# Performance work log

Hardware: AMD Instinct MI355X
Metric: run time of the kernel (lower is better)

## Reference

```python
import jax, jax.numpy as jnp
import numpy as np

NHEADS = 8
LN_EPS = 1e-5

def _layer_norm(x, g, b):
    mu = jnp.mean(x, axis=-1, keepdims=True)
    var = jnp.mean((x - mu) ** 2, axis=-1, keepdims=True)
    return (x - mu) * jax.lax.rsqrt(var + LN_EPS) * g + b

def setup_inputs() -> dict:
    key = jax.random.key(0)
    ks = jax.random.split(key, 12)
    B, L, D = 8, 1024, 512
    F = 2 * D  # ffn_dim = 2*dim
    std = 0.01  # init_weights: Linear weights ~ N(0, 0.01), biases zero
    inp = {
        'query': jax.random.normal(ks[0], (B, L, D), dtype=jnp.float32),
        'q_mask': jnp.ones((B, L), dtype=jnp.int32),
        'wq': jax.random.normal(ks[1], (D, D), dtype=jnp.float32) * std,
        'bq': jnp.zeros((D,), dtype=jnp.float32),
        'wk': jax.random.normal(ks[2], (D, D), dtype=jnp.float32) * std,
        'bk': jnp.zeros((D,), dtype=jnp.float32),
        'wv': jax.random.normal(ks[3], (D, D), dtype=jnp.float32) * std,
        'bv': jnp.zeros((D,), dtype=jnp.float32),
        'wo': jax.random.normal(ks[4], (D, D), dtype=jnp.float32) * std,
        'bo': jnp.zeros((D,), dtype=jnp.float32),
        'ln1_g': jnp.ones((D,), dtype=jnp.float32),
        'ln1_b': jnp.zeros((D,), dtype=jnp.float32),
        'w1': jax.random.normal(ks[5], (D, F), dtype=jnp.float32) * std,
        'b1': jnp.zeros((F,), dtype=jnp.float32),
        'w2': jax.random.normal(ks[6], (F, D), dtype=jnp.float32) * std,
        'b2': jnp.zeros((D,), dtype=jnp.float32),
        'ln2_g': jnp.ones((D,), dtype=jnp.float32),
        'ln2_b': jnp.zeros((D,), dtype=jnp.float32),
    }
    return inp

def reference(query, q_mask, wq, bq, wk, bk, wv, bv, wo, bo, ln1_g, ln1_b, w1, b1, w2, b2, ln2_g, ln2_b):
    B, L, D = query.shape
    H = NHEADS
    dh = D // H
    residual = query
    # projections (dropout in eval mode -> identity)
    q = query @ wq + bq
    k = query @ wk + bk
    v = query @ wv + bv
    # faithful to torch .view(batch*nheads, -1, dim_head) (no head transpose)
    q = q.reshape(B * H, L, dh)
    k = k.reshape(B * H, L, dh)
    v = v.reshape(B * H, L, dh)
    # faithful to torch mask.repeat(nheads, 1) -> tile along batch dim
    mf = q_mask.astype(jnp.float32)
    qm = jnp.tile(mf, (H, 1))  # [B*H, L]
    km = qm
    mask = qm[:, :, None] * km[:, None, :]  # [B*H, L, L] outer product
    scores = jnp.einsum('bqd,bkd->bqk', q, k) / np.sqrt(dh).astype(np.float32)
    A = jnp.where(mask == 0, 0.0, jnp.exp(scores))  # masked_fill(-inf).exp()
    A_sum = jnp.maximum(jnp.sum(A, axis=-1, keepdims=True), 1.0)
    attn = A / A_sum
    context = jnp.einsum('bqk,bkd->bqd', attn, v).reshape(B, L, H * dh)
    out = context @ wo + bo
    out = _layer_norm(residual + out, ln1_g, ln1_b)
    # positional-wise FFN: Linear -> ReLU -> Linear, residual + LayerNorm
    ffn = jax.nn.relu(out @ w1 + b1) @ w2 + b2
    out2 = _layer_norm(out + ffn, ln2_g, ln2_b)
    return (out2, q_mask, query, query, q_mask)
```

## Files before the change

### kernel.cpp

```cpp
#include <hip/hip_runtime.h>
#include <hip/hip_bf16.h>

typedef __hip_bfloat16 bf16;
typedef __attribute__((ext_vector_type(4))) float f32x4;
typedef __attribute__((ext_vector_type(8))) short s16x8;
typedef __attribute__((ext_vector_type(4))) short s16x4;

#define MFMA(a, b, c) __builtin_amdgcn_mfma_f32_16x16x32_bf16((a), (b), (c), 0, 0, 0)

__device__ __forceinline__ void g2l16(const bf16* g, bf16* l) {
  __builtin_amdgcn_global_load_lds((const __attribute__((address_space(1))) void*)g,
                                   (__attribute__((address_space(3))) void*)l,
                                   16, 0, 0);
}
__device__ __forceinline__ bf16 cvt_bf(float f) { return __float2bfloat16(f); }
__device__ __forceinline__ float bf2f(bf16 h) { return __bfloat162float(h); }

__global__ __launch_bounds__(256)
void prep2_k(const float* __restrict__ query, const int* __restrict__ qmask,
             const float* __restrict__ wq, const float* __restrict__ wk,
             const float* __restrict__ wv, const float* __restrict__ wo,
             const float* __restrict__ w1, const float* __restrict__ w2,
             bf16* __restrict__ wqkvT, bf16* __restrict__ woT,
             bf16* __restrict__ w1T, bf16* __restrict__ w2T,
             bf16* __restrict__ qb, float* __restrict__ out)
{
  __shared__ float tl[32][33];
  const int bid = blockIdx.x;
  if (bid < 2048) {
    const float* W; bf16* Wt; int K, N, tile;
    if (bid < 768)        { int s = bid >> 8; W = s==0?wq:(s==1?wk:wv);
                            Wt = wqkvT + s*262144; K = 512; N = 512; tile = bid & 255; }
    else if (bid < 1024)  { W = wo; Wt = woT; K = 512;  N = 512;  tile = bid - 768; }
    else if (bid < 1536)  { W = w1; Wt = w1T; K = 512;  N = 1024; tile = bid - 1024; }
    else                  { W = w2; Wt = w2T; K = 1024; N = 512;  tile = bid - 1536; }
    const int nx = N >> 5;
    const int n0 = (tile % nx) * 32, k0 = (tile / nx) * 32;
    const int tx = threadIdx.x & 31, ty = threadIdx.x >> 5;
#pragma unroll
    for (int i = 0; i < 32; i += 8)
      tl[ty + i][tx] = W[(size_t)(k0 + ty + i) * N + n0 + tx];
    __syncthreads();
#pragma unroll
    for (int i = 0; i < 32; i += 8)
      Wt[(size_t)(n0 + ty + i) * K + k0 + tx] = cvt_bf(tl[tx][ty + i]);
  } else if (bid < 4096) {
    const int i = (bid - 2048) * 2048 + threadIdx.x * 8;
    float4 a = *(const float4*)(query + i);
    float4 b = *(const float4*)(query + i + 4);
    union { bf16 h[8]; s16x8 v; } u;
    u.h[0] = cvt_bf(a.x); u.h[1] = cvt_bf(a.y); u.h[2] = cvt_bf(a.z); u.h[3] = cvt_bf(a.w);
    u.h[4] = cvt_bf(b.x); u.h[5] = cvt_bf(b.y); u.h[6] = cvt_bf(b.z); u.h[7] = cvt_bf(b.w);
    *(s16x8*)(qb + i) = u.v;
    float* o1 = out + 4202496 + i;
    float* o2 = out + 8396800 + i;
    *(float4*)o1 = a; *(float4*)(o1 + 4) = b;
    *(float4*)o2 = a; *(float4*)(o2 + 4) = b;
  } else {
    const int j = (bid - 4096) * 256 + threadIdx.x;
    const float v = (float)qmask[j];
    out[4194304 + j] = v;
    out[12591104 + j] = v;
  }
}

__global__ __launch_bounds__(256)
void cvt_k(const float* __restrict__ in, bf16* __restrict__ o)
{
  const int i = (blockIdx.x * 256 + threadIdx.x) * 8;
  float4 a = *(const float4*)(in + i);
  float4 b = *(const float4*)(in + i + 4);
  union { bf16 h[8]; s16x8 v; } u;
  u.h[0] = cvt_bf(a.x); u.h[1] = cvt_bf(a.y); u.h[2] = cvt_bf(a.z); u.h[3] = cvt_bf(a.w);
  u.h[4] = cvt_bf(b.x); u.h[5] = cvt_bf(b.y); u.h[6] = cvt_bf(b.z); u.h[7] = cvt_bf(b.w);
  *(s16x8*)(o + i) = u.v;
}

__global__ __launch_bounds__(256)
void wcvt_all_k(const float* __restrict__ wq, const float* __restrict__ wk,
                const float* __restrict__ wv, const float* __restrict__ wo,
                const float* __restrict__ w1, const float* __restrict__ w2,
                bf16* __restrict__ wqkvT, bf16* __restrict__ woT,
                bf16* __restrict__ w1T, bf16* __restrict__ w2T)
{
  __shared__ float tl[32][33];
  const int bid = blockIdx.x;
  const float* W; bf16* Wt; int K, N, tile;
  if (bid < 768)        { int s = bid >> 8; W = s==0?wq:(s==1?wk:wv);
                          Wt = wqkvT + s*262144; K = 512; N = 512; tile = bid & 255; }
  else if (bid < 1024)  { W = wo; Wt = woT; K = 512;  N = 512;  tile = bid - 768; }
  else if (bid < 1536)  { W = w1; Wt = w1T; K = 512;  N = 1024; tile = bid - 1024; }
  else                  { W = w2; Wt = w2T; K = 1024; N = 512;  tile = bid - 1536; }
  const int nx = N >> 5;
  const int n0 = (tile % nx) * 32, k0 = (tile / nx) * 32;
  const int tx = threadIdx.x & 31, ty = threadIdx.x >> 5;
#pragma unroll
  for (int i = 0; i < 32; i += 8)
    tl[ty + i][tx] = W[(size_t)(k0 + ty + i) * N + n0 + tx];
  __syncthreads();
#pragma unroll
  for (int i = 0; i < 32; i += 8)
    Wt[(size_t)(n0 + ty + i) * K + k0 + tx] = cvt_bf(tl[tx][ty + i]);
}

template<int BN, int EPI>
__global__ __launch_bounds__(256, 2)
void gemm_k(const bf16* __restrict__ A, const bf16* __restrict__ Bt,
            const float* __restrict__ b0, const float* __restrict__ b1,
            const float* __restrict__ b2,
            const float* __restrict__ rF, const bf16* __restrict__ rB,
            bf16* __restrict__ C0, bf16* __restrict__ C1, bf16* __restrict__ C2,
            int Nout, int K)
{
  constexpr int NI = BN / 32;
  __shared__ bf16 As[128 * 64];
  __shared__ bf16 Bs[BN * 64];
  const int tid = threadIdx.x;
  const int wave = tid >> 6, lane = tid & 63;
  const int g = lane >> 4, c = lane & 15;
  const int wgid = blockIdx.x;
  const int xcd = wgid & 7, idx = wgid >> 3;
  const int m0 = (xcd * 8 + (idx & 7)) * 128;
  const int n0 = (idx >> 3) * BN;
  const int wm = (wave >> 1) * 64, wn = (wave & 1) * (BN / 2);
  const int srl = lane >> 3;
  const int csub = ((lane & 7) ^ (lane >> 3)) * 8;

  f32x4 acc[4][NI];
#pragma unroll
  for (int i = 0; i < 4; ++i)
#pragma unroll
    for (int j = 0; j < NI; ++j) acc[i][j] = (f32x4)0.f;

  for (int k0 = 0; k0 < K; k0 += 64) {
#pragma unroll
    for (int is = 0; is < 4; ++is) {
      const int tr = wave * 32 + is * 8;
      g2l16(A + (size_t)(m0 + tr + srl) * K + (k0 + csub), As + tr * 64);
    }
#pragma unroll
    for (int is = 0; is < BN / 32; ++is) {
      const int tr = wave * (BN / 4) + is * 8;
      g2l16(Bt + (size_t)(n0 + tr + srl) * K + (k0 + csub), Bs + tr * 64);
    }
    __syncthreads();
#pragma unroll
    for (int ks = 0; ks < 2; ++ks) {
      s16x8 af[4], bfr[NI];
#pragma unroll
      for (int i = 0; i < 4; ++i) {
        const int ar = wm + i * 16 + c;
        af[i] = *(const s16x8*)((const char*)As + ar * 128 + ((ks * 4 + g) ^ (ar & 7)) * 16);
      }
#pragma unroll
      for (int i = 0; i < NI; ++i) {
        const int br = wn + i * 16 + c;
        bfr[i] = *(const s16x8*)((const char*)Bs + br * 128 + ((ks * 4 + g) ^ (br & 7)) * 16);
      }
#pragma unroll
      for (int mi = 0; mi < 4; ++mi)
#pragma unroll
        for (int ni = 0; ni < NI; ++ni)
          acc[mi][ni] = MFMA(bfr[ni], af[mi], acc[mi][ni]);
    }
    __syncthreads();
  }

  bf16* Cp; const float* bp; int colbase; int vseg = 0;
  if constexpr (EPI == 0) {
    const int seg = n0 >> 9;
    Cp = seg == 0 ? C0 : (seg == 1 ? C1 : C2);
    bp = seg == 0 ? b0 : (seg == 1 ? b1 : b2);
    colbase = n0 & 511;
    vseg = (seg == 2);
  } else { Cp = C0; bp = b0; colbase = n0; }

#pragma unroll
  for (int mi = 0; mi < 4; ++mi) {
    const int row = m0 + wm + mi * 16 + c;
#pragma unroll
    for (int ni = 0; ni < NI; ++ni) {
      const int colb = colbase + wn + ni * 16 + g * 4;
      f32x4 v = acc[mi][ni];
      const f32x4 bv = *(const f32x4*)(bp + colb);
#pragma unroll
      for (int r = 0; r < 4; ++r) v[r] += bv[r];
      if constexpr (EPI == 1) {
        const f32x4 rv = *(const f32x4*)(rF + (size_t)row * Nout + colb);
#pragma unroll
        for (int r = 0; r < 4; ++r) v[r] += rv[r];
      }
      if constexpr (EPI == 2) {
#pragma unroll
        for (int r = 0; r < 4; ++r) v[r] = fmaxf(v[r], 0.f);
      }
      if constexpr (EPI == 3) {
        union { s16x4 x; bf16 h[4]; } rb;
        rb.x = *(const s16x4*)(rB + (size_t)row * Nout + colb);
#pragma unroll
        for (int r = 0; r < 4; ++r) v[r] += bf2f(rb.h[r]);
      }
      union { bf16 h[4]; s16x4 x; } o;
#pragma unroll
      for (int r = 0; r < 4; ++r) o.h[r] = cvt_bf(v[r]);
      if constexpr (EPI == 0) {
        if (vseg) {
          const int bh = (row >> 10) * 8 + (colb >> 6);
          const int dd = colb & 63, kk2 = row & 1023;
          bf16* vp = Cp + (size_t)bh * 65536 + (size_t)dd * 1024 + kk2;
#pragma unroll
          for (int r = 0; r < 4; ++r) vp[r * 1024] = o.h[r];
        } else {
          *(s16x4*)(Cp + (size_t)row * Nout + colb) = o.x;
        }
      } else {
        *(s16x4*)(Cp + (size_t)row * Nout + colb) = o.x;
      }
    }
  }
}

__global__ __launch_bounds__(256, 2)
void attn_k(const bf16* __restrict__ Q, const bf16* __restrict__ Kp,
            const bf16* __restrict__ Vt, const int* __restrict__ mask,
            bf16* __restrict__ ctx)
{
  __shared__ bf16 Ks[2][64 * 64];
  __shared__ bf16 Vs[2][64 * 64];
  __shared__ __align__(16) float koff[1024];
  const int lane = threadIdx.x & 63, wave = threadIdx.x >> 6;
  const int g = lane >> 4, c = lane & 15;
  const int wg = blockIdx.x;
  const int swz = (wg & 7) * 64 + (wg >> 3);
  const int qb = swz & 7, bh = swz >> 3;
  const int q0w = qb * 128 + wave * 32;
  const bf16* Qg = Q  + (size_t)bh * 65536;
  const bf16* Kg = Kp + (size_t)bh * 65536;
  const bf16* Vg = Vt + (size_t)bh * 65536;
  const int* mrow = mask + (bh & 7) * 1024;

  {
    const int i = threadIdx.x * 4;
    int4 m4 = *(const int4*)(mrow + i);
    f32x4 kv;
    kv[0] = m4.x ? 0.f : -1e30f;
    kv[1] = m4.y ? 0.f : -1e30f;
    kv[2] = m4.z ? 0.f : -1e30f;
    kv[3] = m4.w ? 0.f : -1e30f;
    *(f32x4*)&koff[i] = kv;
  }

  s16x8 qa[2][2];
#pragma unroll
  for (int qs = 0; qs < 2; ++qs)
#pragma unroll
    for (int h = 0; h < 2; ++h)
      qa[qs][h] = *(const s16x8*)(Qg + (size_t)(q0w + qs * 16 + c) * 64 + h * 32 + g * 8);

  float qm[2][4];
#pragma unroll
  for (int qs = 0; qs < 2; ++qs)
#pragma unroll
    for (int r = 0; r < 4; ++r)
      qm[qs][r] = mrow[q0w + qs * 16 + g * 4 + r] ? 1.f : 0.f;

  s16x8 ones;
#pragma unroll
  for (int i = 0; i < 8; ++i) ones[i] = (short)0x3F80;

  f32x4 acc[2][4], asum[2];
#pragma unroll
  for (int qs = 0; qs < 2; ++qs) {
    asum[qs] = (f32x4)0.f;
#pragma unroll
    for (int db = 0; db < 4; ++db) acc[qs][db] = (f32x4)0.f;
  }

  const int rl = lane >> 3, ch = lane & 7;
  const int schunk = (ch ^ rl) * 8;

  auto STAGE = [&](int kt, int buf) {
#pragma unroll
    for (int rnd = 0; rnd < 2; ++rnd) {
      const int rb = wave * 16 + rnd * 8;
      const int l = rb + rl;
      const int i16 = l & 15, kbb = l >> 4;
      const int srow = ((kbb >> 1) << 5) + ((i16 >> 2) << 3) + ((kbb & 1) << 2) + (i16 & 3);
      g2l16(Kg + (size_t)(kt * 64 + srow) * 64 + schunk, &Ks[buf][rb * 64]);
      g2l16(Vg + (size_t)l * 1024 + kt * 64 + schunk, &Vs[buf][rb * 64]);
    }
  };

  STAGE(0, 0);
  __syncthreads();

  for (int kt = 0; kt < 16; ++kt) {
    const int cur = kt & 1;
    if (kt < 15) STAGE(kt + 1, cur ^ 1);

    union { unsigned w[8]; s16x8 v[2]; } pr[2];

#pragma unroll
    for (int kb = 0; kb < 4; ++kb) {
      const int krow = kb * 16 + c;
      const char* kbase = (const char*)&Ks[cur][0] + krow * 128;
      const s16x8 kf0 = *(const s16x8*)(kbase + ((g    ) ^ (c & 7)) * 16);
      const s16x8 kf1 = *(const s16x8*)(kbase + ((g + 4) ^ (c & 7)) * 16);
      const f32x4 ko = *(const f32x4*)&koff[kt * 64 + ((kb >> 1) << 5) + (g << 3) + ((kb & 1) << 2)];
#pragma unroll
      for (int qs = 0; qs < 2; ++qs) {
        f32x4 z = (f32x4)0.f;
        z = MFMA(kf0, qa[qs][0], z);
        z = MFMA(kf1, qa[qs][1], z);
        union { bf16 h[4]; unsigned u[2]; } eh;
#pragma unroll
        for (int r = 0; r < 4; ++r)
          eh.h[r] = cvt_bf(__expf(fmaf(z[r], 0.125f, ko[r])));
        pr[qs].w[kb * 2]     = eh.u[0];
        pr[qs].w[kb * 2 + 1] = eh.u[1];
      }
    }

#pragma unroll
    for (int kk = 0; kk < 2; ++kk) {
      s16x8 vf[4];
#pragma unroll
      for (int db = 0; db < 4; ++db)
        vf[db] = *(const s16x8*)((const char*)&Vs[cur][0] + (db * 16 + c) * 128 + ((4 * kk + g) ^ (c & 7)) * 16);
#pragma unroll
      for (int qs = 0; qs < 2; ++qs) {
        const s16x8 pa = pr[qs].v[kk];
        asum[qs] = MFMA(pa, ones, asum[qs]);
#pragma unroll
        for (int db = 0; db < 4; ++db)
          acc[qs][db] = MFMA(pa, vf[db], acc[qs][db]);
      }
    }
    __syncthreads();
  }

#pragma unroll
  for (int qs = 0; qs < 2; ++qs)
#pragma unroll
    for (int r = 0; r < 4; ++r) {
      const float inv = qm[qs][r] / fmaxf(asum[qs][r], 1.f);
      const size_t qr = q0w + qs * 16 + g * 4 + r;
#pragma unroll
      for (int db = 0; db < 4; ++db)
        ctx[(size_t)bh * 65536 + qr * 64 + db * 16 + c] = cvt_bf(acc[qs][db][r] * inv);
    }
}

template<int INB, int OUTF, int OUTB>
__global__ __launch_bounds__(256)
void ln_k(const void* __restrict__ xin, const float* __restrict__ g,
          const float* __restrict__ bb, float* __restrict__ of, bf16* __restrict__ ob)
{
  const int row = blockIdx.x * 4 + (threadIdx.x >> 6);
  const int lane = threadIdx.x & 63;
  float xv[8];
  if constexpr (INB) {
    union { s16x8 v; bf16 h[8]; } u;
    u.v = *(const s16x8*)((const bf16*)xin + (size_t)row * 512 + lane * 8);
#pragma unroll
    for (int j = 0; j < 8; ++j) xv[j] = bf2f(u.h[j]);
  } else {
    const float* xr = (const float*)xin + (size_t)row * 512 + lane * 8;
    float4 a = *(const float4*)xr, b = *(const float4*)(xr + 4);
    xv[0]=a.x; xv[1]=a.y; xv[2]=a.z; xv[3]=a.w; xv[4]=b.x; xv[5]=b.y; xv[6]=b.z; xv[7]=b.w;
  }
  float s = 0.f, q = 0.f;
#pragma unroll
  for (int j = 0; j < 8; ++j) { s += xv[j]; q += xv[j] * xv[j]; }
#pragma unroll
  for (int m = 1; m < 64; m <<= 1) { s += __shfl_xor(s, m); q += __shfl_xor(q, m); }
  const float mu = s * (1.f / 512.f);
  const float var = q * (1.f / 512.f) - mu * mu;
  const float rs = rsqrtf(var + 1e-5f);
  float4 g0 = *(const float4*)(g + lane * 8),  g1 = *(const float4*)(g + lane * 8 + 4);
  float4 b0 = *(const float4*)(bb + lane * 8), b1 = *(const float4*)(bb + lane * 8 + 4);
  float gv[8] = {g0.x, g0.y, g0.z, g0.w, g1.x, g1.y, g1.z, g1.w};
  float bv[8] = {b0.x, b0.y, b0.z, b0.w, b1.x, b1.y, b1.z, b1.w};
  float ov[8];
#pragma unroll
  for (int j = 0; j < 8; ++j) ov[j] = (xv[j] - mu) * rs * gv[j] + bv[j];
  if constexpr (OUTF) {
    float4 o0 = {ov[0], ov[1], ov[2], ov[3]};
    float4 o1 = {ov[4], ov[5], ov[6], ov[7]};
    float* outr = of + (size_t)row * 512 + lane * 8;
    *(float4*)outr = o0;
    *(float4*)(outr + 4) = o1;
  }
  if constexpr (OUTB) {
    union { bf16 h[8]; s16x8 v; } u;
#pragma unroll
    for (int j = 0; j < 8; ++j) u.h[j] = cvt_bf(ov[j]);
    *(s16x8*)(ob + (size_t)row * 512 + lane * 8) = u.v;
  }
}

__global__ __launch_bounds__(256)
void mask_k(const int* __restrict__ m, float* __restrict__ out)
{
  const int i = blockIdx.x * 256 + threadIdx.x;
  const float v = (float)m[i];
  out[4194304 + i] = v;
  out[12591104 + i] = v;
}

extern "C" void kernel_launch(void* const* d_in, const int* in_sizes, int n_in,
                              void* d_out, int out_size, void* d_ws, size_t ws_size,
                              hipStream_t stream)
{
  const float* query = (const float*)d_in[0];
  const int*   qmask = (const int*)d_in[1];
  const float* wq = (const float*)d_in[2];
  const float* bq = (const float*)d_in[3];
  const float* wk = (const float*)d_in[4];
  const float* bk = (const float*)d_in[5];
  const float* wv = (const float*)d_in[6];
  const float* bv = (const float*)d_in[7];
  const float* wo = (const float*)d_in[8];
  const float* bo = (const float*)d_in[9];
  const float* ln1g = (const float*)d_in[10];
  const float* ln1b = (const float*)d_in[11];
  const float* w1 = (const float*)d_in[12];
  const float* b1 = (const float*)d_in[13];
  const float* w2 = (const float*)d_in[14];
  const float* b2 = (const float*)d_in[15];
  const float* ln2g = (const float*)d_in[16];
  const float* ln2b = (const float*)d_in[17];
  float* out = (float*)d_out;
  char* ws = (char*)d_ws;

  bf16* wqkvT = (bf16*)(ws);
  bf16* woT   = (bf16*)(ws + 1572864);
  bf16* w1T   = (bf16*)(ws + 2097152);
  bf16* w2T   = (bf16*)(ws + 3145728);

  const dim3 blk(256);

  if (ws_size >= (size_t)96468992) {
    bf16*  qb    = (bf16*)(ws + 4194304);
    bf16*  Qb    = (bf16*)(ws + 12582912);
    bf16*  Kb    = (bf16*)(ws + 20971520);
    bf16*  VtG   = (bf16*)(ws + 37748736);
    bf16*  ctx   = (bf16*)(ws + 46137344);
    bf16*  attnr = (bf16*)(ws + 54525952);
    bf16*  x1b   = (bf16*)(ws + 62914560);
    bf16*  hbuf  = (bf16*)(ws + 71303168);
    bf16*  ybuf  = (bf16*)(ws + 88080384);

    prep2_k<<<4128, blk, 0, stream>>>(query, qmask, wq, wk, wv, wo, w1, w2,
                                      wqkvT, woT, w1T, w2T, qb, out);
    gemm_k<128, 0><<<768, blk, 0, stream>>>(qb, wqkvT, bq, bk, bv,
        nullptr, nullptr, Qb, Kb, VtG, 512, 512);
    attn_k<<<512, blk, 0, stream>>>(Qb, Kb, VtG, qmask, ctx);
    gemm_k<64, 3><<<512, blk, 0, stream>>>(ctx, woT, bo, nullptr, nullptr,
        nullptr, qb, attnr, nullptr, nullptr, 512, 512);
    ln_k<1, 0, 1><<<2048, blk, 0, stream>>>(attnr, ln1g, ln1b, nullptr, x1b);
    gemm_k<128, 2><<<512, blk, 0, stream>>>(x1b, w1T, b1, nullptr, nullptr,
        nullptr, nullptr, hbuf, nullptr, nullptr, 1024, 512);
    gemm_k<64, 3><<<512, blk, 0, stream>>>(hbuf, w2T, b2, nullptr, nullptr,
        nullptr, x1b, ybuf, nullptr, nullptr, 512, 1024);
    ln_k<1, 1, 0><<<2048, blk, 0, stream>>>(ybuf, ln2g, ln2b, out, nullptr);
  } else {
    char* ob = (char*)d_out;
    char* R0 = ob;
    char* R1 = ob + 16809984;
    char* R2 = ob + 33587200;
    bf16*  qb    = (bf16*)R0;
    bf16*  ctx   = (bf16*)R0;
    bf16*  x1b   = (bf16*)R0;
    bf16*  Qb    = (bf16*)R1;
    bf16*  Kb    = (bf16*)(R1 + 8388608);
    bf16*  attnr = (bf16*)R1;
    bf16*  hbuf  = (bf16*)R1;
    bf16*  VtG   = (bf16*)(R2 + 8388608);
    bf16*  ybuf  = (bf16*)R2;

    wcvt_all_k<<<2048, blk, 0, stream>>>(wq, wk, wv, wo, w1, w2, wqkvT, woT, w1T, w2T);
    cvt_k<<<2048, blk, 0, stream>>>(query, qb);
    gemm_k<128, 0><<<768, blk, 0, stream>>>(qb, wqkvT, bq, bk, bv,
        nullptr, nullptr, Qb, Kb, VtG, 512, 512);
    attn_k<<<512, blk, 0, stream>>>(Qb, Kb, VtG, qmask, ctx);
    gemm_k<64, 1><<<512, blk, 0, stream>>>(ctx, woT, bo, nullptr, nullptr,
        query, nullptr, attnr, nullptr, nullptr, 512, 512);
    ln_k<1, 0, 1><<<2048, blk, 0, stream>>>(attnr, ln1g, ln1b, nullptr, x1b);
    gemm_k<128, 2><<<512, blk, 0, stream>>>(x1b, w1T, b1, nullptr, nullptr,
        nullptr, nullptr, hbuf, nullptr, nullptr, 1024, 512);
    gemm_k<64, 3><<<512, blk, 0, stream>>>(hbuf, w2T, b2, nullptr, nullptr,
        nullptr, x1b, ybuf, nullptr, nullptr, 512, 1024);
    ln_k<1, 1, 0><<<2048, blk, 0, stream>>>(ybuf, ln2g, ln2b, out, nullptr);
    mask_k<<<32, blk, 0, stream>>>(qmask, out);
    hipMemcpyAsync(out + 4202496, query, 16777216, hipMemcpyDeviceToDevice, stream);
    hipMemcpyAsync(out + 8396800, query, 16777216, hipMemcpyDeviceToDevice, stream);
  }
}
```

Baseline: 215.6 us.

## Fuse output-projection and FFN2 GEMMs with residual add and LayerNorm

```diff
diff --git a/kernel.cpp b/kernel.cpp
--- a/kernel.cpp
+++ b/kernel.cpp
@@ -215,6 +215,124 @@
         }
       } else {
         *(s16x4*)(Cp + (size_t)row * Nout + colb) = o.x;
+      }
+    }
+  }
+}
+
+template<int OUTF>
+__global__ __launch_bounds__(512, 1)
+void gemmln_k(const bf16* __restrict__ A, const bf16* __restrict__ Bt,
+              const float* __restrict__ bias, const bf16* __restrict__ resid,
+              const float* __restrict__ gamma, const float* __restrict__ beta,
+              bf16* __restrict__ outb, float* __restrict__ outf, int K)
+{
+  __shared__ bf16 As[32 * 64];
+  __shared__ bf16 Bs[512 * 64];
+  __shared__ float redS[2][8][16], redQ[2][8][16];
+  const int tid = threadIdx.x;
+  const int wave = tid >> 6, lane = tid & 63;
+  const int g = lane >> 4, c = lane & 15;
+  const int bid = blockIdx.x;
+  const int xcd = bid & 7, idx = bid >> 3;
+  const int m0 = (xcd * 32 + idx) * 32;
+  const int wn = wave * 64;
+  const int rl = lane >> 3;
+  const int csub = ((lane & 7) ^ rl) * 8;
+
+  f32x4 acc[2][4];
+#pragma unroll
+  for (int i = 0; i < 2; ++i)
+#pragma unroll
+    for (int j = 0; j < 4; ++j) acc[i][j] = (f32x4)0.f;
+
+  for (int k0 = 0; k0 < K; k0 += 64) {
+    if (wave < 4)
+      g2l16(A + (size_t)(m0 + wave * 8 + rl) * K + (k0 + csub), As + wave * 8 * 64);
+#pragma unroll
+    for (int is = 0; is < 8; ++is) {
+      const int tr = wn + is * 8;
+      g2l16(Bt + (size_t)(tr + rl) * K + (k0 + csub), Bs + tr * 64);
+    }
+    __syncthreads();
+#pragma unroll
+    for (int ks = 0; ks < 2; ++ks) {
+      s16x8 af[2], bfr[4];
+#pragma unroll
+      for (int i = 0; i < 2; ++i) {
+        const int ar = i * 16 + c;
+        af[i] = *(const s16x8*)((const char*)As + ar * 128 + ((ks * 4 + g) ^ (ar & 7)) * 16);
+      }
+#pragma unroll
+      for (int i = 0; i < 4; ++i) {
+        const int br = wn + i * 16 + c;
+        bfr[i] = *(const s16x8*)((const char*)Bs + br * 128 + ((ks * 4 + g) ^ (br & 7)) * 16);
+      }
+#pragma unroll
+      for (int mi = 0; mi < 2; ++mi)
+#pragma unroll
+        for (int ni = 0; ni < 4; ++ni)
+          acc[mi][ni] = MFMA(bfr[ni], af[mi], acc[mi][ni]);
+    }
+    __syncthreads();
+  }
+
+  float vv[2][4][4];
+  float sP[2], qP[2];
+#pragma unroll
+  for (int mi = 0; mi < 2; ++mi) {
+    sP[mi] = 0.f; qP[mi] = 0.f;
+    const int row = m0 + mi * 16 + c;
+#pragma unroll
+    for (int ni = 0; ni < 4; ++ni) {
+      const int colb = wn + ni * 16 + g * 4;
+      const f32x4 bv = *(const f32x4*)(bias + colb);
+      union { s16x4 x; bf16 h[4]; } rb;
+      rb.x = *(const s16x4*)(resid + (size_t)row * 512 + colb);
+#pragma unroll
+      for (int r = 0; r < 4; ++r) {
+        const float v = acc[mi][ni][r] + bv[r] + bf2f(rb.h[r]);
+        vv[mi][ni][r] = v;
+        sP[mi] += v;
+        qP[mi] += v * v;
+      }
+    }
+    sP[mi] += __shfl_xor(sP[mi], 16); qP[mi] += __shfl_xor(qP[mi], 16);
+    sP[mi] += __shfl_xor(sP[mi], 32); qP[mi] += __shfl_xor(qP[mi], 32);
+  }
+  if (g == 0) {
+#pragma unroll
+    for (int mi = 0; mi < 2; ++mi) { redS[mi][wave][c] = sP[mi]; redQ[mi][wave][c] = qP[mi]; }
+  }
+  __syncthreads();
+
+#pragma unroll
+  for (int mi = 0; mi < 2; ++mi) {
+    float s = 0.f, q = 0.f;
+#pragma unroll
+    for (int w = 0; w < 8; ++w) { s += redS[mi][w][c]; q += redQ[mi][w][c]; }
+    const float mu = s * (1.f / 512.f);
+    const float var = q * (1.f / 512.f) - mu * mu;
+    const float rs = rsqrtf(var + 1e-5f);
+    const int row = m0 + mi * 16 + c;
+#pragma unroll
+    for (int ni = 0; ni < 4; ++ni) {
+      const int colb = wn + ni * 16 + g * 4;
+      const f32x4 g4 = *(const f32x4*)(gamma + colb);
+      const f32x4 b4 = *(const f32x4*)(beta + colb);
+      if constexpr (OUTF) {
+        float4 o;
+        o.x = (vv[mi][ni][0] - mu) * rs * g4[0] + b4[0];
+        o.y = (vv[mi][ni][1] - mu) * rs * g4[1] + b4[1];
+        o.z = (vv[mi][ni][2] - mu) * rs * g4[2] + b4[2];
+        o.w = (vv[mi][ni][3] - mu) * rs * g4[3] + b4[3];
+        *(float4*)(outf + (size_t)row * 512 + colb) = o;
+      } else {
+        union { bf16 h[4]; s16x4 x; } o;
+#pragma unroll
+        for (int r = 0; r < 4; ++r)
+          o.h[r] = cvt_bf((vv[mi][ni][r] - mu) * rs * g4[r] + b4[r]);
+        *(s16x4*)(outb + (size_t)row * 512 + colb) = o.x;
       }
     }
   }
@@ -446,24 +564,20 @@
     bf16*  Kb    = (bf16*)(ws + 20971520);
     bf16*  VtG   = (bf16*)(ws + 37748736);
     bf16*  ctx   = (bf16*)(ws + 46137344);
-    bf16*  attnr = (bf16*)(ws + 54525952);
     bf16*  x1b   = (bf16*)(ws + 62914560);
     bf16*  hbuf  = (bf16*)(ws + 71303168);
-    bf16*  ybuf  = (bf16*)(ws + 88080384);
 
     prep2_k<<<4128, blk, 0, stream>>>(query, qmask, wq, wk, wv, wo, w1, w2,
                                       wqkvT, woT, w1T, w2T, qb, out);
     gemm_k<128, 0><<<768, blk, 0, stream>>>(qb, wqkvT, bq, bk, bv,
         nullptr, nullptr, Qb, Kb, VtG, 512, 512);
     attn_k<<<512, blk, 0, stream>>>(Qb, Kb, VtG, qmask, ctx);
-    gemm_k<64, 3><<<512, blk, 0, stream>>>(ctx, woT, bo, nullptr, nullptr,
-        nullptr, qb, attnr, nullptr, nullptr, 512, 512);
-    ln_k<1, 0, 1><<<2048, blk, 0, stream>>>(attnr, ln1g, ln1b, nullptr, x1b);
+    gemmln_k<0><<<256, dim3(512), 0, stream>>>(ctx, woT, bo, qb, ln1g, ln1b,
+                                               x1b, nullptr, 512);
     gemm_k<128, 2><<<512, blk, 0, stream>>>(x1b, w1T, b1, nullptr, nullptr,
         nullptr, nullptr, hbuf, nullptr, nullptr, 1024, 512);
-    gemm_k<64, 3><<<512, blk, 0, stream>>>(hbuf, w2T, b2, nullptr, nullptr,
-        nullptr, x1b, ybuf, nullptr, nullptr, 512, 1024);
-    ln_k<1, 1, 0><<<2048, blk, 0, stream>>>(ybuf, ln2g, ln2b, out, nullptr);
+    gemmln_k<1><<<256, dim3(512), 0, stream>>>(hbuf, w2T, b2, x1b, ln2g, ln2b,
+                                               nullptr, out, 1024);
   } else {
     char* ob = (char*)d_out;
     char* R0 = ob;
```

Result: slower. 222.1 us (+3.0%).
